# Performance work log

Hardware: AMD Instinct MI355X
Metric: run time of the kernel (lower is better)

## Reference

```python
import jax, jax.numpy as jnp
import numpy as np

K_DIM = 1024
HEADS = 16


def setup_inputs() -> dict:
    key = jax.random.key(0)
    ks = jax.random.split(key, 8)
    b, t, tc, k = 2, 2048, 2048, K_DIM
    scale = 1.0 / np.sqrt(k)
    x = jax.random.normal(ks[0], (b, t, k), dtype=jnp.float32)
    context = jax.random.normal(ks[1], (b, tc, k), dtype=jnp.float32)
    Wq = jax.random.normal(ks[2], (k, k), dtype=jnp.float32) * scale
    Wk = jax.random.normal(ks[3], (k, k), dtype=jnp.float32) * scale
    Wv = jax.random.normal(ks[4], (k, k), dtype=jnp.float32) * scale
    Wo = jax.random.normal(ks[5], (k, k), dtype=jnp.float32) * scale
    bo = jax.random.normal(ks[6], (k,), dtype=jnp.float32) * 0.01
    return {"x": x, "context": context, "Wq": Wq, "Wk": Wk, "Wv": Wv, "Wo": Wo, "bo": bo}


def reference(x, context, Wq, Wk, Wv, Wo, bo):
    b, t, e = x.shape
    tc = context.shape[1]
    h = HEADS
    s = e // h
    # Linear(k,k,bias=False): y = x @ W.T
    q = (x @ Wq.T).reshape(b, t, h, s)
    k_ = (context @ Wk.T).reshape(b, tc, h, s)
    v = (context @ Wv.T).reshape(b, tc, h, s)
    # scale q and k each by e**-0.25 (net 1/sqrt(e), note: full embed dim, not head dim)
    inv4 = e ** (-0.25)
    q = q * inv4
    k_ = k_ * inv4
    # scores: [b, h, t, tc]
    dot = jnp.einsum('bthd,bchd->bhtc', q, k_)
    attn = jax.nn.softmax(dot, axis=-1)
    out = jnp.einsum('bhtc,bchd->bthd', attn, v).reshape(b, t, e)
    return out @ Wo.T + bo
```

## Files before the change

### kernel.cpp

```cpp
#include <hip/hip_runtime.h>
#include <stdint.h>

typedef unsigned short u16;
typedef unsigned int u32;
typedef __attribute__((ext_vector_type(4))) float f32x4;
typedef __attribute__((ext_vector_type(16))) float f32x16;
typedef __attribute__((ext_vector_type(8))) __bf16 bf16x8;
typedef __attribute__((ext_vector_type(8))) u16 u16x8;

constexpr int NB = 2, NT = 2048, NTC = 2048, NE = 1024, NH = 16, ND = 64;
constexpr int MTOK = NB * NT;
constexpr int KDIM = NE;
constexpr float QK_SCALE = (float)(0.17677669529663687 * 1.2011224087864498);
constexpr float FIXED_M = 24.0f;

__device__ __forceinline__ u16 f2bf(float f) {
  union { float f; uint32_t u; } v; v.f = f;
  uint32_t r = v.u + 0x7FFFu + ((v.u >> 16) & 1u);
  return (u16)(r >> 16);
}

__device__ __forceinline__ float fexp2(float x) {
#if __has_builtin(__builtin_amdgcn_exp2f)
  return __builtin_amdgcn_exp2f(x);
#else
  return exp2f(x);
#endif
}

__device__ __forceinline__ u32 cvtpk(float lo, float hi) {
  u32 r;
  asm("v_cvt_pk_bf16_f32 %0, %1, %2" : "=v"(r) : "v"(lo), "v"(hi));
  return r;
}

__device__ __forceinline__ void plswap(u32& a, u32& b) {
  asm("v_permlane32_swap_b32 %0, %1" : "+v"(a), "+v"(b));
}

__device__ __forceinline__ void gload16(const void* g, void* lds) {
  __builtin_amdgcn_global_load_lds(
      (const __attribute__((address_space(1))) unsigned int*)g,
      (__attribute__((address_space(3))) unsigned int*)lds, 16, 0, 0);
}

__device__ __forceinline__ f32x4 mfma16x16(bf16x8 a, bf16x8 b, f32x4 c) {
  return __builtin_amdgcn_mfma_f32_16x16x32_bf16(a, b, c, 0, 0, 0);
}
__device__ __forceinline__ f32x16 mfma32x32(bf16x8 a, bf16x8 b, f32x16 c) {
  return __builtin_amdgcn_mfma_f32_32x32x16_bf16(a, b, c, 0, 0, 0);
}

__device__ __forceinline__ int swz(int row, int part) {
  return row * 128 + ((part ^ (row & 7)) << 4);
}

__device__ __forceinline__ u16x8 cast8(const float4* p, float scale) {
  float4 a = p[0], b = p[1];
  u16x8 r;
  r[0] = f2bf(a.x * scale); r[1] = f2bf(a.y * scale);
  r[2] = f2bf(a.z * scale); r[3] = f2bf(a.w * scale);
  r[4] = f2bf(b.x * scale); r[5] = f2bf(b.y * scale);
  r[6] = f2bf(b.z * scale); r[7] = f2bf(b.w * scale);
  return r;
}

__global__ void cast_all(const float* __restrict__ x, const float* __restrict__ ctx,
                         const float* __restrict__ Wq, const float* __restrict__ Wk,
                         const float* __restrict__ Wv, const float* __restrict__ Wo,
                         u16* __restrict__ xb, u16* __restrict__ cb,
                         u16* __restrict__ wb) {
  int i = blockIdx.x * blockDim.x + threadIdx.x;
  const float* src; u16* dst; int j; float scale = 1.0f;
  if (i < 524288) { src = x; dst = xb; j = i; }
  else if (i < 1048576) { src = ctx; dst = cb; j = i - 524288; }
  else {
    int k = i - 1048576;
    int which = k >> 17; j = k & 131071;
    src = (which == 0) ? Wq : (which == 1) ? Wk : (which == 2) ? Wv : Wo;
    scale = (which < 2) ? QK_SCALE : 1.0f;
    dst = wb + (size_t)which * (NE * KDIM);
  }
  *((u16x8*)dst + j) = cast8((const float4*)src + (size_t)j * 2, scale);
}

__device__ __forceinline__ void gemm_loop(const char* Ab, const char* Bb,
                                          u16* Al, u16* Bl, int tid,
                                          f32x4 (&acc)[2][4]) {
  const int w = tid >> 6, l = tid & 63;
  const int l15 = l & 15, l4 = l >> 4;
  const int wm = w >> 1, wn = w & 1;

  auto stage = [&](int buf, int k0) {
#pragma unroll
    for (int s = 0; s < 2; ++s) {
      int i = (w * 2 + s) * 64 + l;
      int row = i >> 3, part = i & 7;
      int gofs = row * (KDIM * 2) + k0 * 2 + ((part ^ (row & 7)) << 4);
      gload16(Ab + gofs, (char*)(Al + buf * 4096) + (w * 2 + s) * 1024);
    }
#pragma unroll
    for (int s = 0; s < 4; ++s) {
      int i = (w * 4 + s) * 64 + l;
      int row = i >> 3, part = i & 7;
      int gofs = row * (KDIM * 2) + k0 * 2 + ((part ^ (row & 7)) << 4);
      gload16(Bb + gofs, (char*)(Bl + buf * 8192) + (w * 4 + s) * 1024);
    }
  };

  stage(0, 0);
  stage(1, 64);

  for (int it = 0; it < 16; ++it) {
    const int cur = it & 1;
    if (it < 15) asm volatile("s_waitcnt vmcnt(6)" ::: "memory");
    else         asm volatile("s_waitcnt vmcnt(0)" ::: "memory");
    __builtin_amdgcn_s_barrier();
    const char* Ac = (const char*)(Al + cur * 4096);
    const char* Bc = (const char*)(Bl + cur * 8192);
#pragma unroll
    for (int kc = 0; kc < 2; ++kc) {
      bf16x8 af[2], bfr[4];
#pragma unroll
      for (int mt = 0; mt < 2; ++mt)
        af[mt] = *(const bf16x8*)(Ac + swz(wm * 32 + mt * 16 + l15, kc * 4 + l4));
#pragma unroll
      for (int nt = 0; nt < 4; ++nt)
        bfr[nt] = *(const bf16x8*)(Bc + swz(wn * 64 + nt * 16 + l15, kc * 4 + l4));
#pragma unroll
      for (int mt = 0; mt < 2; ++mt)
#pragma unroll
        for (int nt = 0; nt < 4; ++nt)
          acc[mt][nt] = mfma16x16(af[mt], bfr[nt], acc[mt][nt]);
    }
    __builtin_amdgcn_s_barrier();
    if (it < 14) stage(cur, (it + 2) * 64);
  }
}

__global__ __launch_bounds__(256)
void gemm_qkv(const u16* __restrict__ xb, const u16* __restrict__ cb,
              const u16* __restrict__ wqb, const u16* __restrict__ wkvb,
              u16* __restrict__ Qb, u16* __restrict__ KVb) {
  __shared__ __align__(16) u16 Al[2][64 * 64];
  __shared__ __align__(16) u16 Bl[2][128 * 64];
  const int tid = threadIdx.x, w = tid >> 6, l = tid & 63;
  const int l15 = l & 15, l4 = l >> 4;
  const int wm = w >> 1, wn = w & 1;

  int bid = blockIdx.x;
  bid = (bid & 7) * 192 + (bid >> 3);
  const bool isQ = bid < 512;
  const u16* A; const u16* Bm; int mbase, nbase;
  if (isQ) { A = xb; Bm = wqb; nbase = (bid & 7) * 128; mbase = (bid >> 3) * 64; }
  else { int b2 = bid - 512; A = cb; Bm = wkvb; nbase = (b2 & 15) * 128; mbase = (b2 >> 4) * 64; }

  f32x4 acc[2][4] = {};
  gemm_loop((const char*)(A + (size_t)mbase * KDIM),
            (const char*)(Bm + (size_t)nbase * KDIM),
            &Al[0][0], &Bl[0][0], tid, acc);

#pragma unroll
  for (int mt = 0; mt < 2; ++mt) {
#pragma unroll
    for (int nt = 0; nt < 4; ++nt) {
      int col = nbase + wn * 64 + nt * 16 + l15;
      int mrow0 = mbase + wm * 32 + mt * 16 + l4 * 4;
#pragma unroll
      for (int r = 0; r < 4; ++r) {
        int m = mrow0 + r;
        float v = acc[mt][nt][r];
        if (isQ) {
          int b = m >> 11, t = m & (NT - 1), h = col >> 6, d = col & (ND - 1);
          Qb[((size_t)(b * NH + h) * NT + t) * ND + d] = f2bf(v);
        } else {
          int b = m >> 11, tc = m & (NTC - 1);
          int h = (col >> 6) & 15, d = col & (ND - 1);
          size_t base = ((size_t)((b * NH + h) * 32 + (tc >> 6))) * 4096;
          if (col < 1024) {
            size_t idx = base + (size_t)(d >> 3) * 512 + (size_t)(tc & 63) * 8 + (d & 7);
            KVb[idx] = f2bf(v);
          } else {
            size_t idx = base + (size_t)((tc & 63) >> 3) * 512 + (size_t)d * 8 + (tc & 7);
            KVb[4194304 + idx] = f2bf(v);
          }
        }
      }
    }
  }
}

__global__ __launch_bounds__(256)
void gemm_out(const u16* __restrict__ A, const u16* __restrict__ Bm,
              float* __restrict__ Cout, const float* __restrict__ bias) {
  __shared__ __align__(16) u16 Al[2][64 * 64];
  __shared__ __align__(16) u16 Bl[2][128 * 64];
  const int tid = threadIdx.x, w = tid >> 6, l = tid & 63;
  const int l15 = l & 15, l4 = l >> 4;
  const int wm = w >> 1, wn = w & 1;

  int bid = blockIdx.x;
  bid = (bid & 7) * 64 + (bid >> 3);
  const int mbase = (bid >> 3) * 64, nbase = (bid & 7) * 128;

  f32x4 acc[2][4] = {};
  gemm_loop((const char*)(A + (size_t)mbase * KDIM),
            (const char*)(Bm + (size_t)nbase * KDIM),
            &Al[0][0], &Bl[0][0], tid, acc);

#pragma unroll
  for (int mt = 0; mt < 2; ++mt) {
#pragma unroll
    for (int nt = 0; nt < 4; ++nt) {
      int col = nbase + wn * 64 + nt * 16 + l15;
      int mrow0 = mbase + wm * 32 + mt * 16 + l4 * 4;
#pragma unroll
      for (int r = 0; r < 4; ++r)
        Cout[(size_t)(mrow0 + r) * NE + col] = acc[mt][nt][r] + bias[col];
    }
  }
}

__global__ __launch_bounds__(128, 2)
void attn_fwd(const u16* __restrict__ Q, const u16* __restrict__ K,
              const u16* __restrict__ Vt, u16* __restrict__ O) {
  __shared__ float Ol[64 * 64];
  __shared__ float Ll[64];
  const int tid = threadIdx.x, wid = tid >> 6, l = tid & 63;
  const int l31 = l & 31, hi = l >> 5;

  int n = blockIdx.x;
  int work = (n & 7) * 128 + (n >> 3);
  const int bh = work >> 5, qx = work & 31;
  const int b = bh >> 4, h = bh & 15;
  const int qbase = qx * 64;

  const char* Kb = (const char*)(K + (size_t)bh * 32 * 4096);
  const char* Vb = (const char*)(Vt + (size_t)bh * 32 * 4096);
  const u16* Qb = Q + (size_t)bh * NT * ND;

  auto kaddr = [&](int t32, int kc) {
    return Kb + (size_t)(t32 >> 1) * 8192 + (size_t)(kc * 2 + hi) * 1024
              + (size_t)((t32 & 1) * 32 + l31) * 16;
  };
  auto vaddr = [&](int t32, int j) {
    return Vb + (size_t)(t32 >> 1) * 8192
              + (size_t)((t32 & 1) * 4 + (j >> 1) * 2 + hi) * 1024
              + (size_t)((j & 1) * 32 + l31) * 16;
  };

  bf16x8 qf[2][4];
#pragma unroll
  for (int qt = 0; qt < 2; ++qt)
#pragma unroll
    for (int kc = 0; kc < 4; ++kc)
      qf[qt][kc] = *(const bf16x8*)(Qb + (size_t)(qbase + qt * 32 + l31) * ND + kc * 16 + hi * 8);

  f32x16 oacc[2][2] = {};
  f32x16 lacc[2] = {};
  f32x16 minit;
#pragma unroll
  for (int r = 0; r < 16; ++r) minit[r] = -FIXED_M;

  const int tbase = wid * 32;

  bf16x8 kfA[4], kfB[4], vf[4];
#pragma unroll
  for (int kc = 0; kc < 4; ++kc) kfA[kc] = *(const bf16x8*)kaddr(tbase, kc);

  for (int it2 = 0; it2 < 16; ++it2) {
    const int tA = tbase + it2 * 2, tB = tA + 1;

#pragma unroll
    for (int j = 0; j < 4; ++j) vf[j] = *(const bf16x8*)vaddr(tA, j);
#pragma unroll
    for (int kc = 0; kc < 4; ++kc) kfB[kc] = *(const bf16x8*)kaddr(tB, kc);
#pragma unroll
    for (int qt = 0; qt < 2; ++qt) {
      f32x16 sv = minit;
#pragma unroll
      for (int kc = 0; kc < 4; ++kc) sv = mfma32x32(kfA[kc], qf[qt][kc], sv);
#pragma unroll
      for (int r = 0; r < 16; ++r) { sv[r] = fexp2(sv[r]); lacc[qt][r] += sv[r]; }
      bf16x8 pa0, pa1;
      {
        u32 a1 = cvtpk(sv[0], sv[1]), b1 = cvtpk(sv[4], sv[5]);
        u32 a2 = cvtpk(sv[2], sv[3]), b2 = cvtpk(sv[6], sv[7]);
        plswap(a1, b1); plswap(a2, b2);
        u32 a3 = cvtpk(sv[8], sv[9]), b3 = cvtpk(sv[12], sv[13]);
        u32 a4 = cvtpk(sv[10], sv[11]), b4 = cvtpk(sv[14], sv[15]);
        plswap(a3, b3); plswap(a4, b4);
        union { u32 u[4]; bf16x8 v; } ua, ub;
        ua.u[0] = a1; ua.u[1] = a2; ua.u[2] = b1; ua.u[3] = b2;
        ub.u[0] = a3; ub.u[1] = a4; ub.u[2] = b3; ub.u[3] = b4;
        pa0 = ua.v; pa1 = ub.v;
      }
      oacc[qt][0] = mfma32x32(pa0, vf[0], oacc[qt][0]);
      oacc[qt][1] = mfma32x32(pa0, vf[1], oacc[qt][1]);
      oacc[qt][0] = mfma32x32(pa1, vf[2], oacc[qt][0]);
      oacc[qt][1] = mfma32x32(pa1, vf[3], oacc[qt][1]);
    }

#pragma unroll
    for (int j = 0; j < 4; ++j) vf[j] = *(const bf16x8*)vaddr(tB, j);
#pragma unroll
    for (int kc = 0; kc < 4; ++kc) kfA[kc] = *(const bf16x8*)kaddr(tB + 1, kc);
#pragma unroll
    for (int qt = 0; qt < 2; ++qt) {
      f32x16 sv = minit;
#pragma unroll
      for (int kc = 0; kc < 4; ++kc) sv = mfma32x32(kfB[kc], qf[qt][kc], sv);
#pragma unroll
      for (int r = 0; r < 16; ++r) { sv[r] = fexp2(sv[r]); lacc[qt][r] += sv[r]; }
      bf16x8 pa0, pa1;
      {
        u32 a1 = cvtpk(sv[0], sv[1]), b1 = cvtpk(sv[4], sv[5]);
        u32 a2 = cvtpk(sv[2], sv[3]), b2 = cvtpk(sv[6], sv[7]);
        plswap(a1, b1); plswap(a2, b2);
        u32 a3 = cvtpk(sv[8], sv[9]), b3 = cvtpk(sv[12], sv[13]);
        u32 a4 = cvtpk(sv[10], sv[11]), b4 = cvtpk(sv[14], sv[15]);
        plswap(a3, b3); plswap(a4, b4);
        union { u32 u[4]; bf16x8 v; } ua, ub;
        ua.u[0] = a1; ua.u[1] = a2; ua.u[2] = b1; ua.u[3] = b2;
        ub.u[0] = a3; ub.u[1] = a4; ub.u[2] = b3; ub.u[3] = b4;
        pa0 = ua.v; pa1 = ub.v;
      }
      oacc[qt][0] = mfma32x32(pa0, vf[0], oacc[qt][0]);
      oacc[qt][1] = mfma32x32(pa0, vf[1], oacc[qt][1]);
      oacc[qt][0] = mfma32x32(pa1, vf[2], oacc[qt][0]);
      oacc[qt][1] = mfma32x32(pa1, vf[3], oacc[qt][1]);
    }
  }

  float lsum[2];
#pragma unroll
  for (int qt = 0; qt < 2; ++qt) {
    f32x16 t = lacc[qt];
#pragma unroll
    for (int s = 8; s >= 1; s >>= 1)
#pragma unroll
      for (int r = 0; r < s; ++r) t[r] += t[r + s];
    lsum[qt] = t[0] + __shfl_xor(t[0], 32);
  }

  if (wid == 1) {
#pragma unroll
    for (int qt = 0; qt < 2; ++qt) {
#pragma unroll
      for (int r = 0; r < 16; ++r) {
        int crow = (r & 3) + 8 * (r >> 2) + 4 * hi;
        Ol[(qt * 32 + crow) * 64 + l31] = oacc[qt][0][r];
        Ol[(qt * 32 + crow) * 64 + 32 + l31] = oacc[qt][1][r];
      }
      if (!hi) Ll[qt * 32 + l31] = lsum[qt];
    }
  }
  __syncthreads();
  if (wid == 0) {
#pragma unroll
    for (int qt = 0; qt < 2; ++qt) {
      float inv = 1.0f / (lsum[qt] + Ll[qt * 32 + l31]);
#pragma unroll
      for (int r = 0; r < 16; ++r) {
        int crow = (r & 3) + 8 * (r >> 2) + 4 * hi;
        float ir = __shfl(inv, crow);
        int t = qbase + qt * 32 + crow;
        size_t rowo = (size_t)(b * NT + t) * NE + h * 64 + l31;
        O[rowo] = f2bf((oacc[qt][0][r] + Ol[(qt * 32 + crow) * 64 + l31]) * ir);
        O[rowo + 32] = f2bf((oacc[qt][1][r] + Ol[(qt * 32 + crow) * 64 + 32 + l31]) * ir);
      }
    }
  }
}

extern "C" void kernel_launch(void* const* d_in, const int* in_sizes, int n_in,
                              void* d_out, int out_size, void* d_ws, size_t ws_size,
                              hipStream_t stream) {
  const float* x   = (const float*)d_in[0];
  const float* ctx = (const float*)d_in[1];
  const float* Wq  = (const float*)d_in[2];
  const float* Wk  = (const float*)d_in[3];
  const float* Wv  = (const float*)d_in[4];
  const float* Wo  = (const float*)d_in[5];
  const float* bo  = (const float*)d_in[6];
  float* out = (float*)d_out;
  char* ws = (char*)d_ws;

  u16* xb  = (u16*)(ws);
  u16* cb  = (u16*)(ws + (8u  << 20));
  u16* wqb = (u16*)(ws + (16u << 20));
  u16* wkb = (u16*)(ws + (18u << 20));
  u16* wob = (u16*)(ws + (22u << 20));
  u16* Qb  = (u16*)(ws + (24u << 20));
  u16* Kb  = (u16*)(ws + (32u << 20));
  u16* Vtb = (u16*)(ws + (40u << 20));
  u16* Ob  = (u16*)(ws + (48u << 20));

  cast_all<<<6144, 256, 0, stream>>>(x, ctx, Wq, Wk, Wv, Wo, xb, cb, wqb);
  gemm_qkv<<<1536, 256, 0, stream>>>(xb, cb, wqb, wkb, Qb, Kb);
  attn_fwd<<<1024, 128, 0, stream>>>(Qb, Kb, Vtb, Ob);
  gemm_out<<<512, 256, 0, stream>>>(Ob, wob, out, bo);
}
```

Before: 112.9 us.

## Use k-group-major operand layout and 128x128 tiles with 32x32 MFMA in GEMMs

The cast kernel now writes activations and weights in a k-group-major layout (8-element k chunks contiguous per row), and the attention output is written in the same layout. The GEMMs switch from 64x128 tiles with 16x16x32 MFMA to 128x128 tiles with 32x32x16 MFMA, loading each k-group slice without swizzling. The aim is more operand reuse per block and fewer, larger MFMA ops. In exchange the software pipeline is dropped: there is a single LDS buffer with syncthreads around each stage, so loads no longer overlap compute, and grid sizes are halved.

```diff
diff --git a/kernel.cpp b/kernel.cpp
--- a/kernel.cpp
+++ b/kernel.cpp
@@ -44,15 +44,8 @@
       (__attribute__((address_space(3))) unsigned int*)lds, 16, 0, 0);
 }
 
-__device__ __forceinline__ f32x4 mfma16x16(bf16x8 a, bf16x8 b, f32x4 c) {
-  return __builtin_amdgcn_mfma_f32_16x16x32_bf16(a, b, c, 0, 0, 0);
-}
 __device__ __forceinline__ f32x16 mfma32x32(bf16x8 a, bf16x8 b, f32x16 c) {
   return __builtin_amdgcn_mfma_f32_32x32x16_bf16(a, b, c, 0, 0, 0);
-}
-
-__device__ __forceinline__ int swz(int row, int part) {
-  return row * 128 + ((part ^ (row & 7)) << 4);
 }
 
 __device__ __forceinline__ u16x8 cast8(const float4* p, float scale) {
@@ -65,76 +58,66 @@
   return r;
 }
 
+
 __global__ void cast_all(const float* __restrict__ x, const float* __restrict__ ctx,
                          const float* __restrict__ Wq, const float* __restrict__ Wk,
                          const float* __restrict__ Wv, const float* __restrict__ Wo,
                          u16* __restrict__ xb, u16* __restrict__ cb,
-                         u16* __restrict__ wb) {
+                         u16* __restrict__ wqb, u16* __restrict__ wkvb,
+                         u16* __restrict__ wob) {
   int i = blockIdx.x * blockDim.x + threadIdx.x;
-  const float* src; u16* dst; int j; float scale = 1.0f;
-  if (i < 524288) { src = x; dst = xb; j = i; }
-  else if (i < 1048576) { src = ctx; dst = cb; j = i - 524288; }
+  const float* src; u16* dst; int n, kgp, Rr, noff = 0; float scale = 1.0f;
+  int region = i >> 18;
+  if (region == 0) { int j = i; n = j & 4095; kgp = j >> 12; src = x; dst = xb; Rr = 4096; }
+  else if (region == 1) { int j = i & 262143; n = j & 4095; kgp = j >> 12; src = ctx; dst = cb; Rr = 4096; }
   else {
-    int k = i - 1048576;
-    int which = k >> 17; j = k & 131071;
-    src = (which == 0) ? Wq : (which == 1) ? Wk : (which == 2) ? Wv : Wo;
-    scale = (which < 2) ? QK_SCALE : 1.0f;
-    dst = wb + (size_t)which * (NE * KDIM);
-  }
-  *((u16x8*)dst + j) = cast8((const float4*)src + (size_t)j * 2, scale);
-}
-
-__device__ __forceinline__ void gemm_loop(const char* Ab, const char* Bb,
-                                          u16* Al, u16* Bl, int tid,
-                                          f32x4 (&acc)[2][4]) {
+    int j = i & 262143;
+    int wsel = j >> 16, jj = j & 65535;
+    n = jj & 1023; kgp = jj >> 10;
+    src = (wsel == 0) ? Wq : (wsel == 1) ? Wk : (wsel == 2) ? Wv : Wo;
+    scale = (wsel < 2) ? QK_SCALE : 1.0f;
+    if (wsel == 0) { dst = wqb; Rr = 1024; }
+    else if (wsel == 3) { dst = wob; Rr = 1024; }
+    else { dst = wkvb; Rr = 2048; noff = (wsel == 2) ? 1024 : 0; }
+  }
+  const float4* p = (const float4*)(src + (size_t)n * 1024 + kgp * 16);
+  u16x8 g0 = cast8(p, scale);
+  u16x8 g1 = cast8(p + 2, scale);
+  int kg = kgp * 2;
+  *(u16x8*)(dst + ((size_t)kg * Rr + n + noff) * 8) = g0;
+  *(u16x8*)(dst + ((size_t)(kg + 1) * Rr + n + noff) * 8) = g1;
+}
+
+__device__ __forceinline__ void gemm128_loop(const char* Ag, const char* Bg,
+                                             int RrA, int RrB,
+                                             u16* Al, u16* Bl, int tid,
+                                             f32x16 (&acc)[2][2]) {
   const int w = tid >> 6, l = tid & 63;
-  const int l15 = l & 15, l4 = l >> 4;
+  const int l31 = l & 31, hi = l >> 5;
   const int wm = w >> 1, wn = w & 1;
 
-  auto stage = [&](int buf, int k0) {
-#pragma unroll
-    for (int s = 0; s < 2; ++s) {
-      int i = (w * 2 + s) * 64 + l;
-      int row = i >> 3, part = i & 7;
-      int gofs = row * (KDIM * 2) + k0 * 2 + ((part ^ (row & 7)) << 4);
-      gload16(Ab + gofs, (char*)(Al + buf * 4096) + (w * 2 + s) * 1024);
-    }
+  for (int it = 0; it < 16; ++it) {
 #pragma unroll
     for (int s = 0; s < 4; ++s) {
-      int i = (w * 4 + s) * 64 + l;
-      int row = i >> 3, part = i & 7;
-      int gofs = row * (KDIM * 2) + k0 * 2 + ((part ^ (row & 7)) << 4);
-      gload16(Bb + gofs, (char*)(Bl + buf * 8192) + (w * 4 + s) * 1024);
-    }
-  };
-
-  stage(0, 0);
-  stage(1, 64);
-
-  for (int it = 0; it < 16; ++it) {
-    const int cur = it & 1;
-    if (it < 15) asm volatile("s_waitcnt vmcnt(6)" ::: "memory");
-    else         asm volatile("s_waitcnt vmcnt(0)" ::: "memory");
-    __builtin_amdgcn_s_barrier();
-    const char* Ac = (const char*)(Al + cur * 4096);
-    const char* Bc = (const char*)(Bl + cur * 8192);
-#pragma unroll
-    for (int kc = 0; kc < 2; ++kc) {
-      bf16x8 af[2], bfr[4];
-#pragma unroll
-      for (int mt = 0; mt < 2; ++mt)
-        af[mt] = *(const bf16x8*)(Ac + swz(wm * 32 + mt * 16 + l15, kc * 4 + l4));
-#pragma unroll
-      for (int nt = 0; nt < 4; ++nt)
-        bfr[nt] = *(const bf16x8*)(Bc + swz(wn * 64 + nt * 16 + l15, kc * 4 + l4));
-#pragma unroll
-      for (int mt = 0; mt < 2; ++mt)
-#pragma unroll
-        for (int nt = 0; nt < 4; ++nt)
-          acc[mt][nt] = mfma16x16(af[mt], bfr[nt], acc[mt][nt]);
-    }
-    __builtin_amdgcn_s_barrier();
-    if (it < 14) stage(cur, (it + 2) * 64);
+      int g = (w * 4 + s) * 64 + l;
+      int p = g >> 7, rr = g & 127;
+      gload16(Ag + ((size_t)(it * 8 + p) * RrA + rr) * 16, (char*)Al + (w * 4 + s) * 1024);
+      gload16(Bg + ((size_t)(it * 8 + p) * RrB + rr) * 16, (char*)Bl + (w * 4 + s) * 1024);
+    }
+    __syncthreads();
+#pragma unroll
+    for (int kc = 0; kc < 4; ++kc) {
+      const int p = kc * 2 + hi;
+      bf16x8 af0 = *(const bf16x8*)((const char*)Al + (size_t)(p * 128 + wm * 64 + l31) * 16);
+      bf16x8 af1 = *(const bf16x8*)((const char*)Al + (size_t)(p * 128 + wm * 64 + 32 + l31) * 16);
+      bf16x8 bf0 = *(const bf16x8*)((const char*)Bl + (size_t)(p * 128 + wn * 64 + l31) * 16);
+      bf16x8 bf1 = *(const bf16x8*)((const char*)Bl + (size_t)(p * 128 + wn * 64 + 32 + l31) * 16);
+      acc[0][0] = mfma32x32(af0, bf0, acc[0][0]);
+      acc[0][1] = mfma32x32(af0, bf1, acc[0][1]);
+      acc[1][0] = mfma32x32(af1, bf0, acc[1][0]);
+      acc[1][1] = mfma32x32(af1, bf1, acc[1][1]);
+    }
+    __syncthreads();
   }
 }
 
@@ -142,42 +125,43 @@
 void gemm_qkv(const u16* __restrict__ xb, const u16* __restrict__ cb,
               const u16* __restrict__ wqb, const u16* __restrict__ wkvb,
               u16* __restrict__ Qb, u16* __restrict__ KVb) {
-  __shared__ __align__(16) u16 Al[2][64 * 64];
-  __shared__ __align__(16) u16 Bl[2][128 * 64];
+  __shared__ __align__(16) u16 Al[1024 * 8];
+  __shared__ __align__(16) u16 Bl[1024 * 8];
   const int tid = threadIdx.x, w = tid >> 6, l = tid & 63;
-  const int l15 = l & 15, l4 = l >> 4;
+  const int l31 = l & 31, hi = l >> 5;
   const int wm = w >> 1, wn = w & 1;
 
   int bid = blockIdx.x;
-  bid = (bid & 7) * 192 + (bid >> 3);
-  const bool isQ = bid < 512;
-  const u16* A; const u16* Bm; int mbase, nbase;
-  if (isQ) { A = xb; Bm = wqb; nbase = (bid & 7) * 128; mbase = (bid >> 3) * 64; }
-  else { int b2 = bid - 512; A = cb; Bm = wkvb; nbase = (b2 & 15) * 128; mbase = (b2 >> 4) * 64; }
-
-  f32x4 acc[2][4] = {};
-  gemm_loop((const char*)(A + (size_t)mbase * KDIM),
-            (const char*)(Bm + (size_t)nbase * KDIM),
-            &Al[0][0], &Bl[0][0], tid, acc);
+  bid = (bid & 7) * 96 + (bid >> 3);
+  const bool isQ = bid < 256;
+  const u16* A; const u16* Bm; int mbase, nbase, RrB;
+  if (isQ) { A = xb; Bm = wqb; RrB = 1024; nbase = (bid & 7) * 128; mbase = (bid >> 3) * 128; }
+  else { int b2 = bid - 256; A = cb; Bm = wkvb; RrB = 2048;
+         nbase = (b2 & 15) * 128; mbase = (b2 >> 4) * 128; }
+
+  f32x16 acc[2][2] = {};
+  gemm128_loop((const char*)A + (size_t)mbase * 16,
+               (const char*)Bm + (size_t)nbase * 16,
+               4096, RrB, Al, Bl, tid, acc);
 
 #pragma unroll
   for (int mt = 0; mt < 2; ++mt) {
 #pragma unroll
-    for (int nt = 0; nt < 4; ++nt) {
-      int col = nbase + wn * 64 + nt * 16 + l15;
-      int mrow0 = mbase + wm * 32 + mt * 16 + l4 * 4;
-#pragma unroll
-      for (int r = 0; r < 4; ++r) {
-        int m = mrow0 + r;
+    for (int nt = 0; nt < 2; ++nt) {
+      int n = nbase + wn * 64 + nt * 32 + l31;
+#pragma unroll
+      for (int r = 0; r < 16; ++r) {
+        int crow = (r & 3) + 8 * (r >> 2) + 4 * hi;
+        int m = mbase + wm * 64 + mt * 32 + crow;
         float v = acc[mt][nt][r];
         if (isQ) {
-          int b = m >> 11, t = m & (NT - 1), h = col >> 6, d = col & (ND - 1);
+          int b = m >> 11, t = m & (NT - 1), h = n >> 6, d = n & (ND - 1);
           Qb[((size_t)(b * NH + h) * NT + t) * ND + d] = f2bf(v);
         } else {
           int b = m >> 11, tc = m & (NTC - 1);
-          int h = (col >> 6) & 15, d = col & (ND - 1);
+          int h = (n >> 6) & 15, d = n & (ND - 1);
           size_t base = ((size_t)((b * NH + h) * 32 + (tc >> 6))) * 4096;
-          if (col < 1024) {
+          if (n < 1024) {
             size_t idx = base + (size_t)(d >> 3) * 512 + (size_t)(tc & 63) * 8 + (d & 7);
             KVb[idx] = f2bf(v);
           } else {
@@ -193,30 +177,33 @@
 __global__ __launch_bounds__(256)
 void gemm_out(const u16* __restrict__ A, const u16* __restrict__ Bm,
               float* __restrict__ Cout, const float* __restrict__ bias) {
-  __shared__ __align__(16) u16 Al[2][64 * 64];
-  __shared__ __align__(16) u16 Bl[2][128 * 64];
+  __shared__ __align__(16) u16 Al[1024 * 8];
+  __shared__ __align__(16) u16 Bl[1024 * 8];
   const int tid = threadIdx.x, w = tid >> 6, l = tid & 63;
-  const int l15 = l & 15, l4 = l >> 4;
+  const int l31 = l & 31, hi = l >> 5;
   const int wm = w >> 1, wn = w & 1;
 
   int bid = blockIdx.x;
-  bid = (bid & 7) * 64 + (bid >> 3);
-  const int mbase = (bid >> 3) * 64, nbase = (bid & 7) * 128;
-
-  f32x4 acc[2][4] = {};
-  gemm_loop((const char*)(A + (size_t)mbase * KDIM),
-            (const char*)(Bm + (size_t)nbase * KDIM),
-            &Al[0][0], &Bl[0][0], tid, acc);
+  bid = (bid & 7) * 32 + (bid >> 3);
+  const int mbase = (bid >> 3) * 128, nbase = (bid & 7) * 128;
+
+  f32x16 acc[2][2] = {};
+  gemm128_loop((const char*)A + (size_t)mbase * 16,
+               (const char*)Bm + (size_t)nbase * 16,
+               4096, 1024, Al, Bl, tid, acc);
 
 #pragma unroll
   for (int mt = 0; mt < 2; ++mt) {
 #pragma unroll
-    for (int nt = 0; nt < 4; ++nt) {
-      int col = nbase + wn * 64 + nt * 16 + l15;
-      int mrow0 = mbase + wm * 32 + mt * 16 + l4 * 4;
-#pragma unroll
-      for (int r = 0; r < 4; ++r)
-        Cout[(size_t)(mrow0 + r) * NE + col] = acc[mt][nt][r] + bias[col];
+    for (int nt = 0; nt < 2; ++nt) {
+      int n = nbase + wn * 64 + nt * 32 + l31;
+      float bv = bias[n];
+#pragma unroll
+      for (int r = 0; r < 16; ++r) {
+        int crow = (r & 3) + 8 * (r >> 2) + 4 * hi;
+        int m = mbase + wm * 64 + mt * 32 + crow;
+        Cout[(size_t)m * NE + n] = acc[mt][nt][r] + bv;
+      }
     }
   }
 }
@@ -365,9 +352,13 @@
         int crow = (r & 3) + 8 * (r >> 2) + 4 * hi;
         float ir = __shfl(inv, crow);
         int t = qbase + qt * 32 + crow;
-        size_t rowo = (size_t)(b * NT + t) * NE + h * 64 + l31;
-        O[rowo] = f2bf((oacc[qt][0][r] + Ol[(qt * 32 + crow) * 64 + l31]) * ir);
-        O[rowo + 32] = f2bf((oacc[qt][1][r] + Ol[(qt * 32 + crow) * 64 + 32 + l31]) * ir);
+        int token = b * NT + t;
+        float v0 = (oacc[qt][0][r] + Ol[(qt * 32 + crow) * 64 + l31]) * ir;
+        float v1 = (oacc[qt][1][r] + Ol[(qt * 32 + crow) * 64 + 32 + l31]) * ir;
+        size_t i0 = ((size_t)(h * 8 + (l31 >> 3)) * 4096 + token) * 8 + (l31 & 7);
+        size_t i1 = ((size_t)(h * 8 + 4 + (l31 >> 3)) * 4096 + token) * 8 + (l31 & 7);
+        O[i0] = f2bf(v0);
+        O[i1] = f2bf(v1);
       }
     }
   }
@@ -389,15 +380,15 @@
   u16* xb  = (u16*)(ws);
   u16* cb  = (u16*)(ws + (8u  << 20));
   u16* wqb = (u16*)(ws + (16u << 20));
-  u16* wkb = (u16*)(ws + (18u << 20));
+  u16* wkvb= (u16*)(ws + (18u << 20));
   u16* wob = (u16*)(ws + (22u << 20));
   u16* Qb  = (u16*)(ws + (24u << 20));
   u16* Kb  = (u16*)(ws + (32u << 20));
   u16* Vtb = (u16*)(ws + (40u << 20));
   u16* Ob  = (u16*)(ws + (48u << 20));
 
-  cast_all<<<6144, 256, 0, stream>>>(x, ctx, Wq, Wk, Wv, Wo, xb, cb, wqb);
-  gemm_qkv<<<1536, 256, 0, stream>>>(xb, cb, wqb, wkb, Qb, Kb);
+  cast_all<<<3072, 256, 0, stream>>>(x, ctx, Wq, Wk, Wv, Wo, xb, cb, wqb, wkvb, wob);
+  gemm_qkv<<<768, 256, 0, stream>>>(xb, cb, wqb, wkvb, Qb, Kb);
   attn_fwd<<<1024, 128, 0, stream>>>(Qb, Kb, Vtb, Ob);
-  gemm_out<<<512, 256, 0, stream>>>(Ob, wob, out, bo);
-}
+  gemm_out<<<256, 256, 0, stream>>>(Ob, wob, out, bo);
+}
```

After: 125.5 us. 1.11x slower.
